# Kernel tuning notes

Hardware: AMD Instinct MI355X
Metric: run time of the kernel (lower is better)

Reference implementation:

```python
import jax, jax.numpy as jnp
import numpy as np

B, N, M = 8, 4096, 77
Q_DIM, CTX_DIM = 1024, 768
H, D = 16, 64
INNER = H * D  # 1024


def setup_inputs() -> dict:
    key = jax.random.key(0)
    ks = jax.random.split(key, 7)
    x = jax.random.normal(ks[0], (B, N, Q_DIM), dtype=jnp.float32)
    context = jax.random.normal(ks[1], (B, M, CTX_DIM), dtype=jnp.float32)
    # Linear weights stored as [in, out] so y = x @ W (no bias for q/k/v).
    Wq = jax.random.normal(ks[2], (Q_DIM, INNER), dtype=jnp.float32) * (Q_DIM ** -0.5)
    Wk = jax.random.normal(ks[3], (CTX_DIM, INNER), dtype=jnp.float32) * (CTX_DIM ** -0.5)
    Wv = jax.random.normal(ks[4], (CTX_DIM, INNER), dtype=jnp.float32) * (CTX_DIM ** -0.5)
    Wo = jax.random.normal(ks[5], (INNER, Q_DIM), dtype=jnp.float32) * (INNER ** -0.5)
    bo = jax.random.normal(ks[6], (Q_DIM,), dtype=jnp.float32) * 0.01
    return {"x": x, "context": context, "Wq": Wq, "Wk": Wk, "Wv": Wv, "Wo": Wo, "bo": bo}


def reference(x, context, Wq, Wk, Wv, Wo, bo):
    scale = D ** -0.5
    # Project and split heads: [B, S, H*D] -> [B, H, S, D]
    def heads(t):
        b, s, _ = t.shape
        return t.reshape(b, s, H, D).transpose(0, 2, 1, 3)
    q = heads(x @ Wq)        # [B, H, N, D]
    k = heads(context @ Wk)  # [B, H, M, D]
    v = heads(context @ Wv)  # [B, H, M, D]
    scores = jnp.einsum('bhid,bhjd->bhij', q, k) * scale  # [B, H, N, M]
    attn = jax.nn.softmax(scores, axis=-1)
    out = jnp.einsum('bhij,bhjd->bhid', attn, v)          # [B, H, N, D]
    out = out.transpose(0, 2, 1, 3).reshape(x.shape[0], x.shape[1], INNER)
    return out @ Wo + bo  # dropout p=0.0 -> identity
```

## Files before the change

### kernel.cpp

```cpp
#include <hip/hip_runtime.h>
#include <hip/hip_bf16.h>

typedef _Float16 f16x8 __attribute__((ext_vector_type(8)));
typedef float f32x4 __attribute__((ext_vector_type(4)));

#define MFMA16(a, b, c) __builtin_amdgcn_mfma_f32_16x16x32_f16(a, b, c, 0, 0, 0)

__device__ __forceinline__ void load_lds16(const void* g, void* l) {
  __builtin_amdgcn_global_load_lds(
      (__attribute__((address_space(1))) void*)g,
      (__attribute__((address_space(3))) void*)l, 16, 0, 0);
}

__global__ __launch_bounds__(256) void k_prep(const float* __restrict__ x,
                                              const float* __restrict__ ctx,
                                              const float* __restrict__ Wq,
                                              const float* __restrict__ Wk,
                                              const float* __restrict__ Wv,
                                              const float* __restrict__ Wo,
                                              _Float16* __restrict__ xh,
                                              _Float16* __restrict__ ctxh,
                                              _Float16* __restrict__ Wqt,
                                              _Float16* __restrict__ Wkt,
                                              _Float16* __restrict__ Wvt,
                                              _Float16* __restrict__ Wot,
                                              _Float16* __restrict__ Vtg) {
  __shared__ float tile[64][65];
  const int b = blockIdx.x, t = threadIdx.x;

  if (b < 4096) {
    for (int i = b * 256 + t; i < 4194304; i += 4096 * 256) {
      const float4* p = (const float4*)(x + (size_t)i * 8);
      float4 a = p[0], c = p[1];
      f16x8 v = {(_Float16)a.x, (_Float16)a.y, (_Float16)a.z, (_Float16)a.w,
                 (_Float16)c.x, (_Float16)c.y, (_Float16)c.z, (_Float16)c.w};
      *(f16x8*)(xh + (size_t)i * 8) = v;
    }
    return;
  }
  if (b < 4327) {
    int i = (b - 4096) * 256 + t;
    const float4* p = (const float4*)(ctx + (size_t)i * 8);
    float4 a = p[0], c = p[1];
    f16x8 v = {(_Float16)a.x, (_Float16)a.y, (_Float16)a.z, (_Float16)a.w,
               (_Float16)c.x, (_Float16)c.y, (_Float16)c.z, (_Float16)c.w};
    *(f16x8*)(ctxh + (size_t)i * 8) = v;
    return;
  }
  if (b >= 5223) {
    int i = (b - 5223) * 256 + t;
    ((f16x8*)Vtg)[i] = f16x8{};
    return;
  }
  const float* tin;
  _Float16* tout;
  int TK, TN, i;
  if (b < 4583)      { tin = Wq; tout = Wqt; TK = 1024; TN = 1024; i = b - 4327; }
  else if (b < 4775) { tin = Wk; tout = Wkt; TK = 768;  TN = 1024; i = b - 4583; }
  else if (b < 4967) { tin = Wv; tout = Wvt; TK = 768;  TN = 1024; i = b - 4775; }
  else               { tin = Wo; tout = Wot; TK = 1024; TN = 1024; i = b - 4967; }
  int n0 = (i & 15) * 64, k0 = (i >> 4) * 64;
  {
    int nn = t & 63, kb = t >> 6;
#pragma unroll
    for (int s = 0; s < 16; ++s) {
      int kk = kb + s * 4;
      tile[kk][nn] = tin[(size_t)(k0 + kk) * TN + n0 + nn];
    }
  }
  __syncthreads();
  {
    int kk = t & 63, nb = t >> 6;
#pragma unroll
    for (int s = 0; s < 16; ++s) {
      int nn = nb + s * 4;
      tout[(size_t)(n0 + nn) * TK + k0 + kk] = (_Float16)tile[kk][nn];
    }
  }
}

__global__ __launch_bounds__(64) void k_kvproj(const _Float16* __restrict__ ctxh,
                                               const _Float16* __restrict__ Wkt,
                                               const _Float16* __restrict__ Wvt,
                                               _Float16* __restrict__ Kg,
                                               _Float16* __restrict__ Vtg) {
  int mt = blockIdx.x, nt = blockIdx.y;
  int lane = threadIdx.x;
  int l15 = lane & 15, lhi = lane >> 4;
  int arow = mt * 16 + l15;
  if (arow > 615) arow = 615;
  const _Float16* ap = ctxh + (size_t)arow * 768 + lhi * 8;
  const _Float16* kp = Wkt + (size_t)(nt * 16 + l15) * 768 + lhi * 8;
  const _Float16* vp = Wvt + (size_t)(nt * 16 + l15) * 768 + lhi * 8;
  f32x4 ak = {0.f, 0.f, 0.f, 0.f}, av = {0.f, 0.f, 0.f, 0.f};
#pragma unroll 4
  for (int ks = 0; ks < 24; ++ks) {
    f16x8 a = *(const f16x8*)(ap + ks * 32);
    f16x8 bk = *(const f16x8*)(kp + ks * 32);
    f16x8 bv = *(const f16x8*)(vp + ks * 32);
    ak = MFMA16(a, bk, ak);
    av = MFMA16(a, bv, av);
  }
  int n = nt * 16 + l15, h = n >> 6, d = n & 63;
#pragma unroll
  for (int j = 0; j < 4; ++j) {
    int gm = mt * 16 + lhi * 4 + j;
    if (gm < 616) {
      int b = gm / 77, m = gm - b * 77;
      Kg[((size_t)(b * 16 + h) * 77 + m) * 64 + d] = (_Float16)ak[j];
      Vtg[((size_t)(b * 16 + h) * 64 + d) * 128 + m] = (_Float16)av[j];
    }
  }
}

__global__ __launch_bounds__(1024) void k_attn(const _Float16* __restrict__ Qh,
                                               const _Float16* __restrict__ Kg,
                                               const _Float16* __restrict__ Vtg,
                                               _Float16* __restrict__ Out) {
  __shared__ __align__(16) char Kl[80 * 128];
  __shared__ __align__(16) char Vl[64 * 256];
  __shared__ __align__(16) char Pl[16 * 16 * 256];
  int bh = blockIdx.y, b = bh >> 4, h = bh & 15;
  int t = threadIdx.x, wid = t >> 6, lane = t & 63;
  int l15 = lane & 15, lhi = lane >> 4;

  const _Float16* Kgp = Kg + (size_t)bh * (77 * 64);
  const _Float16* Vgp = Vtg + (size_t)bh * (64 * 128);

  for (int idx = t; idx < 640; idx += 1024) {
    int m = idx >> 3, c = (idx & 7) * 8;
    f16x8 v = {};
    if (m < 77) v = *(const f16x8*)(Kgp + m * 64 + c);
    *(f16x8*)(Kl + ((m * 128 + c * 2) ^ ((m & 7) << 4))) = v;
  }
  for (int idx = t; idx < 1024; idx += 1024) {
    int d = idx >> 4, c = (idx & 15) * 8;
    f16x8 v = *(const f16x8*)(Vgp + d * 128 + c);
    *(f16x8*)(Vl + ((d * 256 + c * 2) ^ ((d & 7) << 4))) = v;
  }
  char* myP = Pl + wid * 4096;
#pragma unroll
  for (int i = 0; i < 4; ++i) *(f16x8*)(myP + lane * 64 + i * 16) = f16x8{};
  __syncthreads();

  int qrow = b * 4096 + blockIdx.x * 256 + wid * 16 + l15;
  const _Float16* qp = Qh + (size_t)qrow * 1024 + h * 64 + lhi * 8;
  f16x8 q0 = *(const f16x8*)qp;
  f16x8 q1 = *(const f16x8*)(qp + 32);

  float e[5][4];
  float mx[4] = {-1e30f, -1e30f, -1e30f, -1e30f};
#pragma unroll
  for (int ct = 0; ct < 5; ++ct) {
    int m = ct * 16 + l15;
    int d0b = lhi * 16;
    f16x8 k0 = *(const f16x8*)(Kl + ((m * 128 + d0b) ^ ((m & 7) << 4)));
    f16x8 k1 = *(const f16x8*)(Kl + ((m * 128 + 64 + d0b) ^ ((m & 7) << 4)));
    f32x4 acc = {0.f, 0.f, 0.f, 0.f};
    acc = MFMA16(q0, k0, acc);
    acc = MFMA16(q1, k1, acc);
    bool valid = m < 77;
#pragma unroll
    for (int j = 0; j < 4; ++j) {
      float v = valid ? acc[j] * 0.125f : -1e30f;
      e[ct][j] = v;
      mx[j] = fmaxf(mx[j], v);
    }
  }
#pragma unroll
  for (int off = 1; off < 16; off <<= 1)
#pragma unroll
    for (int j = 0; j < 4; ++j) mx[j] = fmaxf(mx[j], __shfl_xor(mx[j], off, 64));
  float sm[4] = {0.f, 0.f, 0.f, 0.f};
#pragma unroll
  for (int ct = 0; ct < 5; ++ct)
#pragma unroll
    for (int j = 0; j < 4; ++j) {
      float ev = __expf(e[ct][j] - mx[j]);
      e[ct][j] = ev;
      sm[j] += ev;
    }
#pragma unroll
  for (int off = 1; off < 16; off <<= 1)
#pragma unroll
    for (int j = 0; j < 4; ++j) sm[j] += __shfl_xor(sm[j], off, 64);
  float rs[4];
#pragma unroll
  for (int j = 0; j < 4; ++j) rs[j] = 1.0f / sm[j];

#pragma unroll
  for (int ct = 0; ct < 5; ++ct) {
    int m = ct * 16 + l15;
#pragma unroll
    for (int j = 0; j < 4; ++j) {
      int r = lhi * 4 + j;
      *(_Float16*)(myP + ((r * 256 + m * 2) ^ ((r & 7) << 4))) =
          (_Float16)(e[ct][j] * rs[j]);
    }
  }

  f32x4 o[4] = {{0.f,0.f,0.f,0.f},{0.f,0.f,0.f,0.f},{0.f,0.f,0.f,0.f},{0.f,0.f,0.f,0.f}};
#pragma unroll
  for (int ks = 0; ks < 3; ++ks) {
    int m0b = ks * 64 + lhi * 16;
    f16x8 pa = *(const f16x8*)(myP + ((l15 * 256 + m0b) ^ ((l15 & 7) << 4)));
#pragma unroll
    for (int dt = 0; dt < 4; ++dt) {
      int d = dt * 16 + l15;
      f16x8 vb = *(const f16x8*)(Vl + ((d * 256 + m0b) ^ ((d & 7) << 4)));
      o[dt] = MFMA16(pa, vb, o[dt]);
    }
  }
  _Float16* op = Out + (size_t)(b * 4096 + blockIdx.x * 256 + wid * 16) * 1024 + h * 64;
#pragma unroll
  for (int dt = 0; dt < 4; ++dt)
#pragma unroll
    for (int j = 0; j < 4; ++j) {
      int r = lhi * 4 + j;
      op[(size_t)r * 1024 + dt * 16 + l15] = (_Float16)o[dt][j];
    }
}

template <int FINAL>
__global__ __launch_bounds__(512, 2) void k_gemm7(const _Float16* __restrict__ A,
                                                  const _Float16* __restrict__ Bt,
                                                  void* __restrict__ Cout,
                                                  const float* __restrict__ bias,
                                                  int M, int N, int K) {
  __shared__ __align__(16) char lds[131072];
  const int t = threadIdx.x, wid = t >> 6, lane = t & 63;
  const int wr = wid >> 2, wc = wid & 3;
  const int l15 = lane & 15, lhi = lane >> 4;

  int nwg = gridDim.x, bid = blockIdx.x;
  int wg = ((nwg & 7) == 0) ? ((bid & 7) * (nwg >> 3) + (bid >> 3)) : bid;
  const int nTN = N >> 8;
  const int tm = wg / nTN, tn = wg % nTN;

  const _Float16* Ag = A + (size_t)tm * 256 * K;
  const _Float16* Bg = Bt + (size_t)tn * 256 * K;
  const size_t stg = (size_t)(wid * 8 + (lane >> 3)) * K +
                     (size_t)(((lane & 7) ^ ((lane >> 3) & 7)) * 8);
  const int dstg = wid * 1024;

  const int x7 = l15 & 7;
  const int cs0 = (lhi ^ x7) << 4;
  const int cs1 = ((4 + lhi) ^ x7) << 4;
  const int aoff = wr * 16384 + l15 * 128;
  const int boff = 32768 + wc * 8192 + l15 * 128;

  f32x4 acc[8][4];
#pragma unroll
  for (int i = 0; i < 8; ++i)
#pragma unroll
    for (int j = 0; j < 4; ++j) acc[i][j] = f32x4{0.f, 0.f, 0.f, 0.f};
  f16x8 a0k0[4], a0k1[4], a1k0[4], a1k1[4];
  f16x8 b00[2], b01[2], b10[2], b11[2];

#define STG_A(T, RB) load_lds16(Ag + stg + (size_t)(RB) * K + (T) * 64, \
                                lds + ((T) & 1) * 65536 + (RB) * 128 + dstg)
#define STG_B(T, RB) load_lds16(Bg + stg + (size_t)(RB) * K + (T) * 64, \
                                lds + ((T) & 1) * 65536 + 32768 + (RB) * 128 + dstg)
#define STG_TILE(T) { STG_A(T, 0); STG_A(T, 64); STG_A(T, 128); STG_A(T, 192);  \
                      STG_B(T, 0); STG_B(T, 64); STG_B(T, 128); STG_B(T, 192); }
#define RDA(DST, BUF, MH, CS) { const int p_ = (BUF) * 65536 + aoff + (MH) * 8192; \
    _Pragma("unroll") for (int mf = 0; mf < 4; ++mf)                               \
      DST[mf] = *(const f16x8*)&lds[p_ + mf * 2048 + (CS)]; }
#define RDB(DST, BUF, NH, CS) { const int q_ = (BUF) * 65536 + boff + (NH) * 4096; \
    _Pragma("unroll") for (int nf = 0; nf < 2; ++nf)                               \
      DST[nf] = *(const f16x8*)&lds[q_ + nf * 2048 + (CS)]; }
#define MMC(MH, NH, AR, BR) { __builtin_amdgcn_s_setprio(1);                       \
    _Pragma("unroll") for (int mf = 0; mf < 4; ++mf)                               \
      _Pragma("unroll") for (int nf = 0; nf < 2; ++nf)                             \
        acc[(MH)*4+mf][(NH)*2+nf] = MFMA16(AR[mf], BR[nf],                         \
                                           acc[(MH)*4+mf][(NH)*2+nf]);             \
    __builtin_amdgcn_s_setprio(0); }
#define VM0 asm volatile("s_waitcnt vmcnt(0)" ::: "memory")
#define BAR __builtin_amdgcn_s_barrier()

#define TILE(BUF, T, STG_ON)                                                       \
  {                                                                                \
    VM0; BAR;                                                                      \
    RDA(a0k0, BUF, 0, cs0); RDB(b00, BUF, 0, cs0);                                 \
    RDB(b10, BUF, 1, cs0);                                                         \
    if (STG_ON) STG_TILE((T) + 1);                                                 \
    MMC(0, 0, a0k0, b00);                                                          \
    RDA(a1k0, BUF, 1, cs0); MMC(0, 1, a0k0, b10);                                  \
    RDA(a1k1, BUF, 1, cs1); MMC(1, 1, a1k0, b10);                                  \
    RDB(b01, BUF, 0, cs1);  MMC(1, 0, a1k0, b00);                                  \
    RDB(b11, BUF, 1, cs1);  MMC(1, 0, a1k1, b01);                                  \
    RDA(a0k1, BUF, 0, cs1); MMC(1, 1, a1k1, b11);                                  \
    MMC(0, 1, a0k1, b11);                                                          \
    MMC(0, 0, a0k1, b01);                                                          \
  }

  const int nT = K >> 6;

  STG_TILE(0);

  for (int i = 0; i < (nT >> 1) - 1; ++i) {
    TILE(0, 2 * i, true);
    TILE(1, 2 * i + 1, true);
  }
  TILE(0, nT - 2, true);
  TILE(1, nT - 1, false);

  const long rbase = (long)tm * 256 + wr * 128;
  const int cbase = tn * 256 + wc * 64;
#pragma unroll
  for (int mf = 0; mf < 8; ++mf)
#pragma unroll
    for (int nf = 0; nf < 4; ++nf) {
      int c = cbase + nf * 16 + l15;
      float bv = FINAL ? bias[c] : 0.f;
#pragma unroll
      for (int j = 0; j < 4; ++j) {
        long r = rbase + mf * 16 + lhi * 4 + j;
        float v = acc[mf][nf][j];
        if (FINAL) ((float*)Cout)[r * N + c] = v + bv;
        else ((_Float16*)Cout)[r * N + c] = (_Float16)v;
      }
    }
#undef STG_A
#undef STG_B
#undef STG_TILE
#undef RDA
#undef RDB
#undef MMC
#undef TILE
#undef VM0
#undef BAR
}

extern "C" void kernel_launch(void* const* d_in, const int* in_sizes, int n_in,
                              void* d_out, int out_size, void* d_ws, size_t ws_size,
                              hipStream_t stream) {
  const float* x   = (const float*)d_in[0];
  const float* ctx = (const float*)d_in[1];
  const float* Wq  = (const float*)d_in[2];
  const float* Wk  = (const float*)d_in[3];
  const float* Wv  = (const float*)d_in[4];
  const float* Wo  = (const float*)d_in[5];
  const float* bo  = (const float*)d_in[6];

  char* ws = (char*)d_ws;
  _Float16* xh   = (_Float16*)(ws + 0);
  _Float16* Wqt  = (_Float16*)(ws + 67108864);
  _Float16* Wkt  = (_Float16*)(ws + 69206016);
  _Float16* Wvt  = (_Float16*)(ws + 70778880);
  _Float16* Wot  = (_Float16*)(ws + 72351744);
  _Float16* ctxh = (_Float16*)(ws + 74448896);
  _Float16* Kg   = (_Float16*)(ws + 75395072);
  _Float16* Vtg  = (_Float16*)(ws + 76656640);
  _Float16* Qh   = (_Float16*)d_out;

  k_prep<<<5735, 256, 0, stream>>>(x, ctx, Wq, Wk, Wv, Wo,
                                   xh, ctxh, Wqt, Wkt, Wvt, Wot, Vtg);
  k_kvproj<<<dim3(39, 64), 64, 0, stream>>>(ctxh, Wkt, Wvt, Kg, Vtg);
  k_gemm7<0><<<dim3(512), dim3(512), 0, stream>>>(xh, Wqt, (void*)Qh, nullptr, 32768, 1024, 1024);
  k_attn<<<dim3(16, 128), 1024, 0, stream>>>(Qh, Kg, Vtg, xh);
  k_gemm7<1><<<dim3(512), dim3(512), 0, stream>>>(xh, Wot, d_out, bo, 32768, 1024, 1024);
}
```

Before: 260.5 us.

## Fuse cross-attention into the Q-projection GEMM epilogue

Removes the separate attention kernel and computes attention directly in the epilogue of the Q projection GEMM. Each wave's 128x64 accumulator tile, which is one head's slice, is stored to LDS as fp16 Q. Each wave then runs QK^T, softmax and PV against K and V read straight from global memory, writing the attention output into a workspace buffer. This avoids writing the full Q matrix to global memory, reading it back, and paying an extra kernel launch. In exchange, the fused GEMM needs 160KB of LDS, which likely lowers its occupancy, and the attention epilogue runs serially per wave with K/V fetched from global or L2 rather than LDS.

```diff
diff --git a/kernel.cpp b/kernel.cpp
--- a/kernel.cpp
+++ b/kernel.cpp
@@ -113,121 +113,15 @@
   }
 }
 
-__global__ __launch_bounds__(1024) void k_attn(const _Float16* __restrict__ Qh,
-                                               const _Float16* __restrict__ Kg,
-                                               const _Float16* __restrict__ Vtg,
-                                               _Float16* __restrict__ Out) {
-  __shared__ __align__(16) char Kl[80 * 128];
-  __shared__ __align__(16) char Vl[64 * 256];
-  __shared__ __align__(16) char Pl[16 * 16 * 256];
-  int bh = blockIdx.y, b = bh >> 4, h = bh & 15;
-  int t = threadIdx.x, wid = t >> 6, lane = t & 63;
-  int l15 = lane & 15, lhi = lane >> 4;
-
-  const _Float16* Kgp = Kg + (size_t)bh * (77 * 64);
-  const _Float16* Vgp = Vtg + (size_t)bh * (64 * 128);
-
-  for (int idx = t; idx < 640; idx += 1024) {
-    int m = idx >> 3, c = (idx & 7) * 8;
-    f16x8 v = {};
-    if (m < 77) v = *(const f16x8*)(Kgp + m * 64 + c);
-    *(f16x8*)(Kl + ((m * 128 + c * 2) ^ ((m & 7) << 4))) = v;
-  }
-  for (int idx = t; idx < 1024; idx += 1024) {
-    int d = idx >> 4, c = (idx & 15) * 8;
-    f16x8 v = *(const f16x8*)(Vgp + d * 128 + c);
-    *(f16x8*)(Vl + ((d * 256 + c * 2) ^ ((d & 7) << 4))) = v;
-  }
-  char* myP = Pl + wid * 4096;
-#pragma unroll
-  for (int i = 0; i < 4; ++i) *(f16x8*)(myP + lane * 64 + i * 16) = f16x8{};
-  __syncthreads();
-
-  int qrow = b * 4096 + blockIdx.x * 256 + wid * 16 + l15;
-  const _Float16* qp = Qh + (size_t)qrow * 1024 + h * 64 + lhi * 8;
-  f16x8 q0 = *(const f16x8*)qp;
-  f16x8 q1 = *(const f16x8*)(qp + 32);
-
-  float e[5][4];
-  float mx[4] = {-1e30f, -1e30f, -1e30f, -1e30f};
-#pragma unroll
-  for (int ct = 0; ct < 5; ++ct) {
-    int m = ct * 16 + l15;
-    int d0b = lhi * 16;
-    f16x8 k0 = *(const f16x8*)(Kl + ((m * 128 + d0b) ^ ((m & 7) << 4)));
-    f16x8 k1 = *(const f16x8*)(Kl + ((m * 128 + 64 + d0b) ^ ((m & 7) << 4)));
-    f32x4 acc = {0.f, 0.f, 0.f, 0.f};
-    acc = MFMA16(q0, k0, acc);
-    acc = MFMA16(q1, k1, acc);
-    bool valid = m < 77;
-#pragma unroll
-    for (int j = 0; j < 4; ++j) {
-      float v = valid ? acc[j] * 0.125f : -1e30f;
-      e[ct][j] = v;
-      mx[j] = fmaxf(mx[j], v);
-    }
-  }
-#pragma unroll
-  for (int off = 1; off < 16; off <<= 1)
-#pragma unroll
-    for (int j = 0; j < 4; ++j) mx[j] = fmaxf(mx[j], __shfl_xor(mx[j], off, 64));
-  float sm[4] = {0.f, 0.f, 0.f, 0.f};
-#pragma unroll
-  for (int ct = 0; ct < 5; ++ct)
-#pragma unroll
-    for (int j = 0; j < 4; ++j) {
-      float ev = __expf(e[ct][j] - mx[j]);
-      e[ct][j] = ev;
-      sm[j] += ev;
-    }
-#pragma unroll
-  for (int off = 1; off < 16; off <<= 1)
-#pragma unroll
-    for (int j = 0; j < 4; ++j) sm[j] += __shfl_xor(sm[j], off, 64);
-  float rs[4];
-#pragma unroll
-  for (int j = 0; j < 4; ++j) rs[j] = 1.0f / sm[j];
-
-#pragma unroll
-  for (int ct = 0; ct < 5; ++ct) {
-    int m = ct * 16 + l15;
-#pragma unroll
-    for (int j = 0; j < 4; ++j) {
-      int r = lhi * 4 + j;
-      *(_Float16*)(myP + ((r * 256 + m * 2) ^ ((r & 7) << 4))) =
-          (_Float16)(e[ct][j] * rs[j]);
-    }
-  }
-
-  f32x4 o[4] = {{0.f,0.f,0.f,0.f},{0.f,0.f,0.f,0.f},{0.f,0.f,0.f,0.f},{0.f,0.f,0.f,0.f}};
-#pragma unroll
-  for (int ks = 0; ks < 3; ++ks) {
-    int m0b = ks * 64 + lhi * 16;
-    f16x8 pa = *(const f16x8*)(myP + ((l15 * 256 + m0b) ^ ((l15 & 7) << 4)));
-#pragma unroll
-    for (int dt = 0; dt < 4; ++dt) {
-      int d = dt * 16 + l15;
-      f16x8 vb = *(const f16x8*)(Vl + ((d * 256 + m0b) ^ ((d & 7) << 4)));
-      o[dt] = MFMA16(pa, vb, o[dt]);
-    }
-  }
-  _Float16* op = Out + (size_t)(b * 4096 + blockIdx.x * 256 + wid * 16) * 1024 + h * 64;
-#pragma unroll
-  for (int dt = 0; dt < 4; ++dt)
-#pragma unroll
-    for (int j = 0; j < 4; ++j) {
-      int r = lhi * 4 + j;
-      op[(size_t)r * 1024 + dt * 16 + l15] = (_Float16)o[dt][j];
-    }
-}
-
-template <int FINAL>
-__global__ __launch_bounds__(512, 2) void k_gemm7(const _Float16* __restrict__ A,
+template <int MODE>
+__global__ __launch_bounds__(512, 2) void k_gemm9(const _Float16* __restrict__ A,
                                                   const _Float16* __restrict__ Bt,
                                                   void* __restrict__ Cout,
                                                   const float* __restrict__ bias,
+                                                  const _Float16* __restrict__ Kg,
+                                                  const _Float16* __restrict__ Vtg,
                                                   int M, int N, int K) {
-  __shared__ __align__(16) char lds[131072];
+  __shared__ __align__(16) char lds[MODE == 0 ? 163840 : 131072];
   const int t = threadIdx.x, wid = t >> 6, lane = t & 63;
   const int wr = wid >> 2, wc = wid & 3;
   const int l15 = lane & 15, lhi = lane >> 4;
@@ -305,22 +199,126 @@
   TILE(0, nT - 2, true);
   TILE(1, nT - 1, false);
 
-  const long rbase = (long)tm * 256 + wr * 128;
-  const int cbase = tn * 256 + wc * 64;
+  if (MODE == 1) {
+    const long rbase = (long)tm * 256 + wr * 128;
+    const int cbase = tn * 256 + wc * 64;
+#pragma unroll
+    for (int mf = 0; mf < 8; ++mf)
+#pragma unroll
+      for (int nf = 0; nf < 4; ++nf) {
+        int c = cbase + nf * 16 + l15;
+        float bv = bias[c];
+#pragma unroll
+        for (int j = 0; j < 4; ++j) {
+          long r = rbase + mf * 16 + lhi * 4 + j;
+          ((float*)Cout)[r * N + c] = acc[mf][nf][j] + bv;
+        }
+      }
+    return;
+  }
+
+  BAR;
+
+  const int h = tn * 4 + wc;
+  const int bh = (tm >> 4) * 16 + h;
+  const _Float16* Kgp = Kg + (size_t)bh * (77 * 64);
+  const _Float16* Vgp = Vtg + (size_t)bh * (64 * 128);
+
+  const int qbase = wid * 16384;
 #pragma unroll
   for (int mf = 0; mf < 8; ++mf)
 #pragma unroll
-    for (int nf = 0; nf < 4; ++nf) {
-      int c = cbase + nf * 16 + l15;
-      float bv = FINAL ? bias[c] : 0.f;
+    for (int nf = 0; nf < 4; ++nf)
 #pragma unroll
       for (int j = 0; j < 4; ++j) {
-        long r = rbase + mf * 16 + lhi * 4 + j;
-        float v = acc[mf][nf][j];
-        if (FINAL) ((float*)Cout)[r * N + c] = v + bv;
-        else ((_Float16*)Cout)[r * N + c] = (_Float16)v;
-      }
-    }
+        int row = mf * 16 + lhi * 4 + j;
+        int d = nf * 16 + l15;
+        int by = (row * 128 + d * 2) ^ ((row & 7) << 4);
+        *(_Float16*)&lds[qbase + by] = (_Float16)acc[mf][nf][j];
+      }
+
+  const int pbase = 131072 + wid * 4096;
+#pragma unroll
+  for (int i = 0; i < 4; ++i)
+    *(f16x8*)&lds[pbase + lane * 64 + i * 16] = f16x8{};
+
+  const long orow0 = (long)tm * 256 + wr * 128;
+  _Float16* aOut = (_Float16*)Cout;
+
+  for (int mf = 0; mf < 8; ++mf) {
+    const int qm = qbase + mf * 2048 + l15 * 128;
+    f16x8 q0 = *(const f16x8*)&lds[qm + cs0];
+    f16x8 q1 = *(const f16x8*)&lds[qm + cs1];
+
+    float e[5][4];
+    float mx[4] = {-1e30f, -1e30f, -1e30f, -1e30f};
+#pragma unroll
+    for (int ct = 0; ct < 5; ++ct) {
+      int m = ct * 16 + l15;
+      f16x8 k0 = *(const f16x8*)(Kgp + m * 64 + lhi * 8);
+      f16x8 k1 = *(const f16x8*)(Kgp + m * 64 + 32 + lhi * 8);
+      f32x4 s = {0.f, 0.f, 0.f, 0.f};
+      s = MFMA16(q0, k0, s);
+      s = MFMA16(q1, k1, s);
+      bool valid = m < 77;
+#pragma unroll
+      for (int j = 0; j < 4; ++j) {
+        float v = valid ? s[j] * 0.125f : -1e30f;
+        e[ct][j] = v;
+        mx[j] = fmaxf(mx[j], v);
+      }
+    }
+#pragma unroll
+    for (int off = 1; off < 16; off <<= 1)
+#pragma unroll
+      for (int j = 0; j < 4; ++j) mx[j] = fmaxf(mx[j], __shfl_xor(mx[j], off, 64));
+    float sm[4] = {0.f, 0.f, 0.f, 0.f};
+#pragma unroll
+    for (int ct = 0; ct < 5; ++ct)
+#pragma unroll
+      for (int j = 0; j < 4; ++j) {
+        float ev = __expf(e[ct][j] - mx[j]);
+        e[ct][j] = ev;
+        sm[j] += ev;
+      }
+#pragma unroll
+    for (int off = 1; off < 16; off <<= 1)
+#pragma unroll
+      for (int j = 0; j < 4; ++j) sm[j] += __shfl_xor(sm[j], off, 64);
+    float rs[4];
+#pragma unroll
+    for (int j = 0; j < 4; ++j) rs[j] = 1.0f / sm[j];
+
+#pragma unroll
+    for (int ct = 0; ct < 5; ++ct) {
+      int m = ct * 16 + l15;
+#pragma unroll
+      for (int j = 0; j < 4; ++j) {
+        int r = lhi * 4 + j;
+        *(_Float16*)&lds[pbase + ((r * 256 + m * 2) ^ ((r & 7) << 4))] =
+            (_Float16)(e[ct][j] * rs[j]);
+      }
+    }
+
+    f32x4 o[4] = {{0.f,0.f,0.f,0.f},{0.f,0.f,0.f,0.f},{0.f,0.f,0.f,0.f},{0.f,0.f,0.f,0.f}};
+#pragma unroll
+    for (int ks = 0; ks < 3; ++ks) {
+      int m0b = ks * 64 + lhi * 16;
+      f16x8 pa = *(const f16x8*)&lds[pbase + ((l15 * 256 + m0b) ^ ((l15 & 7) << 4))];
+#pragma unroll
+      for (int dt = 0; dt < 4; ++dt) {
+        int d = dt * 16 + l15;
+        f16x8 vb = *(const f16x8*)(Vgp + d * 128 + ks * 32 + lhi * 8);
+        o[dt] = MFMA16(pa, vb, o[dt]);
+      }
+    }
+    _Float16* op = aOut + (size_t)(orow0 + mf * 16 + lhi * 4) * 1024 + h * 64;
+#pragma unroll
+    for (int dt = 0; dt < 4; ++dt)
+#pragma unroll
+      for (int j = 0; j < 4; ++j)
+        op[(size_t)j * 1024 + dt * 16 + l15] = (_Float16)o[dt][j];
+  }
 #undef STG_A
 #undef STG_B
 #undef STG_TILE
@@ -352,12 +350,13 @@
   _Float16* ctxh = (_Float16*)(ws + 74448896);
   _Float16* Kg   = (_Float16*)(ws + 75395072);
   _Float16* Vtg  = (_Float16*)(ws + 76656640);
-  _Float16* Qh   = (_Float16*)d_out;
+  _Float16* aOut = (_Float16*)(ws + 78774272);
 
   k_prep<<<5735, 256, 0, stream>>>(x, ctx, Wq, Wk, Wv, Wo,
                                    xh, ctxh, Wqt, Wkt, Wvt, Wot, Vtg);
   k_kvproj<<<dim3(39, 64), 64, 0, stream>>>(ctxh, Wkt, Wvt, Kg, Vtg);
-  k_gemm7<0><<<dim3(512), dim3(512), 0, stream>>>(xh, Wqt, (void*)Qh, nullptr, 32768, 1024, 1024);
-  k_attn<<<dim3(16, 128), 1024, 0, stream>>>(Qh, Kg, Vtg, xh);
-  k_gemm7<1><<<dim3(512), dim3(512), 0, stream>>>(xh, Wot, d_out, bo, 32768, 1024, 1024);
-}
+  k_gemm9<0><<<dim3(512), dim3(512), 0, stream>>>(xh, Wqt, (void*)aOut, nullptr,
+                                                  Kg, Vtg, 32768, 1024, 1024);
+  k_gemm9<1><<<dim3(512), dim3(512), 0, stream>>>(aOut, Wot, d_out, bo,
+                                                  nullptr, nullptr, 32768, 1024, 1024);
+}
```

New measurement: 245.0 us. 5.9% less time.
